# Kernel tuning notes

Hardware: AMD Instinct MI355X
Metric: run time of the kernel (lower is better)

The kernel has to match this reference:

```python
import jax, jax.numpy as jnp
import numpy as np

D_MODEL, N_HEADS, D_K, D_V, D_FF, N_LAYERS = 512, 8, 64, 64, 2048, 6
NEG = -1e9
EPS = 1e-5


def layernorm(x):
    # nn.LayerNorm(d_model) created fresh each call: weight=1, bias=0
    mu = jnp.mean(x, axis=-1, keepdims=True)
    var = jnp.var(x, axis=-1, keepdims=True)
    return (x - mu) * jax.lax.rsqrt(var + EPS)


def sinusoidal_pe(seq_len, d_model, dtype=jnp.float32):
    pos = np.arange(seq_len)[:, None].astype(np.float64)
    div = np.exp(np.arange(0, d_model, 2).astype(np.float64) * (-np.log(10000.0) / d_model))
    pe = np.zeros((seq_len, d_model))
    pe[:, 0::2] = np.sin(pos * div)
    pe[:, 1::2] = np.cos(pos * div)
    return jnp.asarray(pe, dtype=dtype)


def mha(q_in, k_in, v_in, mask, Wq, Wk, Wv, Wo):
    # q_in: [B,Lq,D]; k_in/v_in: [B,Lk,D]; mask: [B,Lq,Lk] bool (True = masked)
    B, Lq, _ = q_in.shape
    Lk = k_in.shape[1]
    Q = (q_in @ Wq).reshape(B, Lq, N_HEADS, D_K).transpose(0, 2, 1, 3)
    K = (k_in @ Wk).reshape(B, Lk, N_HEADS, D_K).transpose(0, 2, 1, 3)
    V = (v_in @ Wv).reshape(B, Lk, N_HEADS, D_V).transpose(0, 2, 1, 3)
    scores = jnp.einsum('bhqd,bhkd->bhqk', Q, K) / jnp.sqrt(jnp.asarray(D_K, q_in.dtype))
    scores = jnp.where(mask[:, None, :, :], jnp.asarray(NEG, scores.dtype), scores)
    attn = jax.nn.softmax(scores, axis=-1)
    ctx = jnp.einsum('bhqk,bhkd->bhqd', attn, V)
    ctx = ctx.transpose(0, 2, 1, 3).reshape(B, Lq, N_HEADS * D_V)
    return layernorm(ctx @ Wo + q_in)


def setup_inputs() -> dict:
    key = jax.random.key(0)
    ks = jax.random.split(key, 16)
    B, T, S, V = 8, 1024, 1024, 32000
    s = 0.02
    inp = {
        'dec_inputs': jax.random.randint(ks[0], (B, T), 0, V),
        'enc_inputs': jax.random.randint(ks[1], (B, S), 0, V),
        'enc_outputs': jax.random.normal(ks[2], (B, S, D_MODEL), jnp.float32),
        'emb': jax.random.normal(ks[3], (V, D_MODEL), jnp.float32) * s,
        'Wq_self': jax.random.normal(ks[4], (N_LAYERS, D_MODEL, N_HEADS * D_K), jnp.float32) * s,
        'Wk_self': jax.random.normal(ks[5], (N_LAYERS, D_MODEL, N_HEADS * D_K), jnp.float32) * s,
        'Wv_self': jax.random.normal(ks[6], (N_LAYERS, D_MODEL, N_HEADS * D_V), jnp.float32) * s,
        'Wo_self': jax.random.normal(ks[7], (N_LAYERS, N_HEADS * D_V, D_MODEL), jnp.float32) * s,
        'Wq_cross': jax.random.normal(ks[8], (N_LAYERS, D_MODEL, N_HEADS * D_K), jnp.float32) * s,
        'Wk_cross': jax.random.normal(ks[9], (N_LAYERS, D_MODEL, N_HEADS * D_K), jnp.float32) * s,
        'Wv_cross': jax.random.normal(ks[10], (N_LAYERS, D_MODEL, N_HEADS * D_V), jnp.float32) * s,
        'Wo_cross': jax.random.normal(ks[11], (N_LAYERS, N_HEADS * D_V, D_MODEL), jnp.float32) * s,
        'W1': jax.random.normal(ks[12], (N_LAYERS, D_MODEL, D_FF), jnp.float32) * s,
        'W2': jax.random.normal(ks[13], (N_LAYERS, D_FF, D_MODEL), jnp.float32) * s,
    }
    return inp


def reference(dec_inputs, enc_inputs, enc_outputs, emb, Wq_self, Wk_self, Wv_self, Wo_self,
              Wq_cross, Wk_cross, Wv_cross, Wo_cross, W1, W2):
    B, T = dec_inputs.shape
    S = enc_inputs.shape[1]
    # embedding with padding_idx=0 (row 0 forced to zero)
    emb_eff = emb.at[0].set(0.0)
    x = emb_eff[dec_inputs] + sinusoidal_pe(T, D_MODEL, emb.dtype)[None, :, :]
    # masks: True = masked
    pad_self = (dec_inputs == 0)[:, None, :]                       # [B,1,T]
    causal = jnp.triu(jnp.ones((T, T), bool), k=1)[None, :, :]     # [1,T,T]
    self_mask = pad_self | causal                                  # [B,T,T]
    enc_mask = jnp.broadcast_to((enc_inputs == 0)[:, None, :], (B, T, S))

    def layer(x, p):
        wqs, wks, wvs, wos, wqc, wkc, wvc, woc, w1, w2 = p
        x = mha(x, x, x, self_mask, wqs, wks, wvs, wos)
        x = mha(x, enc_outputs, enc_outputs, enc_mask, wqc, wkc, wvc, woc)
        h = jax.nn.relu(x @ w1) @ w2
        return layernorm(h + x), None

    params = (Wq_self, Wk_self, Wv_self, Wo_self, Wq_cross, Wk_cross, Wv_cross, Wo_cross, W1, W2)
    x, _ = jax.lax.scan(layer, x, params)
    return x
```

## Files before the change

kernel.cpp:

```cpp
#include <hip/hip_runtime.h>
#include <hip/hip_bf16.h>

#define DMODEL 512
#define NH     8
#define DHEAD  64
#define DFF    2048
#define NLAYER 6
#define BB     8
#define TT     1024
#define NTOK   (BB*TT)
#define ACTE   ((size_t)NTOK*DMODEL)

#define QSCALE 0.18033688011112042f

#define RESCALE_THR 8.0f

typedef __bf16  bf16x8  __attribute__((ext_vector_type(8)));
typedef float   float4v __attribute__((ext_vector_type(4)));
typedef short   short4v __attribute__((ext_vector_type(4)));
typedef short   short8v __attribute__((ext_vector_type(8)));

__device__ __forceinline__ unsigned short f2bf(float f) {
    __hip_bfloat16 h = __float2bfloat16(f);
    return *reinterpret_cast<unsigned short*>(&h);
}

__device__ __forceinline__ void gl_lds16(const void* g, void* l) {
    __builtin_amdgcn_global_load_lds((const __attribute__((address_space(1))) void*)g,
                                     (__attribute__((address_space(3))) void*)l, 16, 0, 0);
}

__device__ __forceinline__ int sigma64(int x) {
    return (x & 32) | ((x & 12) << 1) | ((x & 16) >> 2) | (x & 3);
}

struct Tr8Args {
    const float* src[8];
    unsigned short* dst[8];
    int dstL[8];
    int rowOff[8];
};
__global__ __launch_bounds__(256) void transpose8_kernel(Tr8Args a)
{
    __shared__ float tile[64][65];
    const int type = blockIdx.z / 6, lyr = blockIdx.z % 6;
    const float* src = a.src[type] + (size_t)lyr * 512 * 512;
    unsigned short* dst = a.dst[type] + (size_t)lyr * a.dstL[type];
    const int rowOff = a.rowOff[type];
    const int k0 = blockIdx.x * 64, n0 = blockIdx.y * 64;
    const int tid = threadIdx.x;
#pragma unroll
    for (int rep = 0; rep < 16; ++rep) {
        int idx = rep * 256 + tid;
        int r = idx >> 6, c = idx & 63;
        tile[r][c] = src[(size_t)(k0 + r) * 512 + n0 + c];
    }
    __syncthreads();
#pragma unroll
    for (int rep = 0; rep < 16; ++rep) {
        int idx = rep * 256 + tid;
        int r = idx >> 6, c = idx & 63;
        dst[(size_t)(rowOff + n0 + r) * 512 + k0 + c] = f2bf(tile[c][r]);
    }
}

__global__ __launch_bounds__(256) void transpose_conv_kernel(
    const float* __restrict__ W, unsigned short* __restrict__ Wt, int K, int N,
    size_t dstL, int rowOff)
{
    __shared__ float tile[64][65];
    const float* src = W + (size_t)blockIdx.z * K * N;
    unsigned short* dst = Wt + (size_t)blockIdx.z * dstL;
    const int k0 = blockIdx.x * 64, n0 = blockIdx.y * 64;
    const int tid = threadIdx.x;
#pragma unroll
    for (int rep = 0; rep < 16; ++rep) {
        int idx = rep * 256 + tid;
        int r = idx >> 6, c = idx & 63;
        tile[r][c] = src[(size_t)(k0 + r) * N + n0 + c];
    }
    __syncthreads();
#pragma unroll
    for (int rep = 0; rep < 16; ++rep) {
        int idx = rep * 256 + tid;
        int r = idx >> 6, c = idx & 63;
        dst[(size_t)(rowOff + n0 + r) * K + k0 + c] = f2bf(tile[c][r]);
    }
}

__global__ __launch_bounds__(256) void conv_bf16_kernel(
    const float* __restrict__ in, unsigned short* __restrict__ o)
{
    int i = (blockIdx.x * 256 + threadIdx.x) * 4;
    float4v v = *(const float4v*)(in + i);
    short4v w;
    w[0] = (short)f2bf(v[0]); w[1] = (short)f2bf(v[1]);
    w[2] = (short)f2bf(v[2]); w[3] = (short)f2bf(v[3]);
    *(short4v*)(o + i) = w;
}

__global__ __launch_bounds__(256) void embed_kernel(
    const int* __restrict__ dec, const float* __restrict__ emb,
    unsigned short* __restrict__ xb)
{
    const int row = blockIdx.x;
    const int t = row & (TT - 1);
    const int tid = threadIdx.x;
    const int tok = dec[row];
#pragma unroll
    for (int rep = 0; rep < 2; ++rep) {
        int c = tid + rep * 256;
        float e = (tok != 0) ? emb[(size_t)tok * DMODEL + c] : 0.f;
        int j = c >> 1;
        float freq = __expf(-(float)(2 * j) * (9.210340371976184f / 512.f));
        float ang = (float)t * freq;
        float pe = (c & 1) ? cosf(ang) : sinf(ang);
        xb[(size_t)row * DMODEL + c] = f2bf(e + pe);
    }
}

__global__ __launch_bounds__(256) void add_ln2(
    const float* __restrict__ t, unsigned short* __restrict__ xb,
    float* __restrict__ xout)
{
    const int lane = threadIdx.x & 63;
    const int row = blockIdx.x * 4 + (threadIdx.x >> 6);
    const size_t idx = (size_t)row * DMODEL + lane * 8;
    float4v t0 = *(const float4v*)(t + idx);
    float4v t1 = *(const float4v*)(t + idx + 4);
    float4v u0 = *(const float4v*)(t + ACTE + idx);
    float4v u1 = *(const float4v*)(t + ACTE + idx + 4);
    bf16x8 rb = *(const bf16x8*)(xb + idx);
    float v[8];
#pragma unroll
    for (int k = 0; k < 4; ++k) {
        v[k] = t0[k] + u0[k] + (float)rb[k];
        v[4 + k] = t1[k] + u1[k] + (float)rb[4 + k];
    }
    float s = 0.f, sq = 0.f;
#pragma unroll
    for (int k = 0; k < 8; ++k) { s += v[k]; sq += v[k] * v[k]; }
#pragma unroll
    for (int o = 1; o < 64; o <<= 1) { s += __shfl_xor(s, o); sq += __shfl_xor(sq, o); }
    float mu = s * (1.f / 512.f);
    float var = sq * (1.f / 512.f) - mu * mu;
    float rstd = rsqrtf(var + 1e-5f);
    if (xout) {
        float4v y0, y1;
#pragma unroll
        for (int k = 0; k < 4; ++k) { y0[k] = (v[k] - mu) * rstd; y1[k] = (v[4 + k] - mu) * rstd; }
        *(float4v*)(xout + idx) = y0;
        *(float4v*)(xout + idx + 4) = y1;
    } else {
        short8v w;
#pragma unroll
        for (int k = 0; k < 8; ++k) w[k] = (short)f2bf((v[k] - mu) * rstd);
        *(short8v*)(xb + idx) = w;
    }
}

template <int EPI, int SPLITK = 1>
__global__ __launch_bounds__(256) void gemm_bt(
    const unsigned short* __restrict__ A,
    const unsigned short* __restrict__ Bt,
    float* __restrict__ Cf,
    unsigned short* __restrict__ Cb,
    int M, int N, int K)
{
    __shared__ __attribute__((aligned(16))) short As[2 * 128 * 32];
    __shared__ __attribute__((aligned(16))) short Bs[2 * 128 * 32];
    const int tid = threadIdx.x;
    const int lane = tid & 63, wv = tid >> 6;
    const int quad = lane >> 4, l15 = lane & 15;
    const int m0 = blockIdx.x * 128, n0 = blockIdx.y * 128;
    const int wm = wv & 1, wn = wv >> 1;

    float4v acc[4][4];
#pragma unroll
    for (int i = 0; i < 4; ++i)
#pragma unroll
        for (int j = 0; j < 4; ++j) acc[i][j] = (float4v){0.f, 0.f, 0.f, 0.f};

    const int Kc = K / SPLITK;
    const int kbeg = (SPLITK > 1) ? (int)blockIdx.z * Kc : 0;
    for (int k0 = kbeg; k0 < kbeg + Kc; k0 += 64) {
#pragma unroll
        for (int c = 0; c < 2; ++c)
#pragma unroll
            for (int i = 0; i < 2; ++i) {
                const int inst = wv * 2 + i;
                const int row = inst * 16 + (lane >> 2);
                const int cb = (lane & 3) ^ ((row >> 1) & 3);
                gl_lds16(A + (size_t)(m0 + row) * K + k0 + c * 32 + cb * 8,
                         (char*)As + c * 8192 + inst * 1024);
                gl_lds16(Bt + (size_t)(n0 + row) * K + k0 + c * 32 + cb * 8,
                         (char*)Bs + c * 8192 + inst * 1024);
            }
        __syncthreads();
#pragma unroll
        for (int c = 0; c < 2; ++c) {
            bf16x8 a[4], b[4];
#pragma unroll
            for (int i = 0; i < 4; ++i) {
                const int r = wm * 64 + i * 16 + l15;
                const int st = quad ^ ((r >> 1) & 3);
                a[i] = *(const bf16x8*)&As[c * 4096 + r * 32 + st * 8];
            }
#pragma unroll
            for (int j = 0; j < 4; ++j) {
                const int r = wn * 64 + j * 16 + l15;
                const int st = quad ^ ((r >> 1) & 3);
                b[j] = *(const bf16x8*)&Bs[c * 4096 + r * 32 + st * 8];
            }
#pragma unroll
            for (int i = 0; i < 4; ++i)
#pragma unroll
                for (int j = 0; j < 4; ++j)
                    acc[i][j] = __builtin_amdgcn_mfma_f32_16x16x32_bf16(a[i], b[j], acc[i][j], 0, 0, 0);
        }
        __syncthreads();
    }

    const size_t zoff = (SPLITK > 1) ? (size_t)blockIdx.z * ACTE : 0;
#pragma unroll
    for (int i = 0; i < 4; ++i) {
        const int row_base = m0 + wm * 64 + i * 16 + quad * 4;
#pragma unroll
        for (int j = 0; j < 4; ++j) {
            const int col = n0 + wn * 64 + j * 16 + l15;
#pragma unroll
            for (int r = 0; r < 4; ++r) {
                const int row = row_base + r;
                const float v = acc[i][j][r];
                if (EPI == 0) {
                    Cf[zoff + (size_t)row * N + col] = v;
                } else if (EPI == 1) {
                    Cb[(size_t)row * N + col] = f2bf(fmaxf(v, 0.f));
                } else if (EPI == 2) {
                    const int which = col >> 9;
                    const float sc = (which == 0) ? QSCALE : 1.f;
                    const int b_ = row >> 10, t = row & (TT - 1);
                    const int h = (col >> 6) & 7, d = col & 63;
                    Cb[(size_t)which * ACTE + (((size_t)(b_ * NH + h)) * TT + t) * DHEAD + d] = f2bf(v * sc);
                } else {
                    const int layer = col >> 10, which = (col >> 9) & 1;
                    const int b_ = row >> 10, t = row & (TT - 1);
                    const int h = (col >> 6) & 7, d = col & 63;
                    Cb[(size_t)(layer * 2 + which) * ACTE +
                       (((size_t)(b_ * NH + h)) * TT + t) * DHEAD + d] = f2bf(v);
                }
            }
        }
    }
}

template <bool CAUSAL, int CHAINS>
__global__ __launch_bounds__(256, (CHAINS == 1 ? 4 : 2)) void attn_kernel(
    const unsigned short* __restrict__ Q,
    const unsigned short* __restrict__ Kb,
    const unsigned short* __restrict__ Vb,
    const int* __restrict__ tokens,
    unsigned short* __restrict__ ctx)
{
    __shared__ __attribute__((aligned(16))) short Ks[2][64 * 64];
    __shared__ __attribute__((aligned(16))) short Vt[2][64 * 64];

    const int tid = threadIdx.x, lane = tid & 63, wv = tid >> 6;
    const int quad = lane >> 4, l15 = lane & 15;
    const int bh = blockIdx.x;
    const int qt0 = CAUSAL ? (15 - (int)blockIdx.y) : (int)blockIdx.y;
    const int qt1 = qt0 + 8;
    const int b = bh >> 3, h = bh & 7;
    const size_t kvbase = (size_t)bh * TT * DHEAD;

    const int qcol = wv * 16 + l15;
    const int qg0 = qt0 * 64 + qcol;
    const int qg1 = qt1 * 64 + qcol;

    const bf16x8 qa0 = *(const bf16x8*)&Q[kvbase + (size_t)qg0 * DHEAD + quad * 8];
    const bf16x8 qa1 = *(const bf16x8*)&Q[kvbase + (size_t)qg0 * DHEAD + 32 + quad * 8];
    bf16x8 qb0, qb1;
    if (CHAINS == 2) {
        qb0 = *(const bf16x8*)&Q[kvbase + (size_t)qg1 * DHEAD + quad * 8];
        qb1 = *(const bf16x8*)&Q[kvbase + (size_t)qg1 * DHEAD + 32 + quad * 8];
    }

    float4v O0[4], O1[4];
#pragma unroll
    for (int j = 0; j < 4; ++j) { O0[j] = (float4v){0.f,0.f,0.f,0.f}; O1[j] = (float4v){0.f,0.f,0.f,0.f}; }
    float m0_ = -INFINITY, l0_ = 0.f, m1_ = -INFINITY, l1_ = 0.f;

    const int sig = sigma64(lane);

    const int key0 = (lane & 31) * 2;
    const int d0 = (lane >> 5) * 8 + wv * 16;
    auto stageK = [&](int kt_, int buf) {
#pragma unroll
        for (int i = 0; i < 2; ++i) {
            const int inst = wv * 2 + i;
            const int row = inst * 8 + (lane >> 3);
            const int cb = (lane & 7) ^ (row & 7);
            gl_lds16(Kb + kvbase + (size_t)(kt_ * 64 + sigma64(row)) * DHEAD + cb * 8,
                     (char*)Ks[buf] + inst * 1024);
        }
    };
    auto loadV = [&](int kt_, short8v& r0, short8v& r1) {
        const unsigned short* vp = Vb + kvbase + (size_t)(kt_ * 64 + key0) * DHEAD + d0;
        r0 = *(const short8v*)vp;
        r1 = *(const short8v*)(vp + DHEAD);
    };
    auto writeV = [&](int buf, const short8v& r0, const short8v& r1) {
        const int kc = key0 >> 3, ko = key0 & 7;
#pragma unroll
        for (int j = 0; j < 8; ++j) {
            const int d = d0 + j;
            unsigned pk = (unsigned)(unsigned short)r0[j] |
                          ((unsigned)(unsigned short)r1[j] << 16);
            *(unsigned*)&Vt[buf][d * 64 + ((kc ^ (d & 7)) << 3) + ko] = pk;
        }
    };

    auto softmax_step = [&](const float4v* st, unsigned long long kbits, bool diag,
                            float& m, float& l, float4v* O, bf16x8& p0, bf16x8& p1) {
        const bool domask = (kbits != 0ull) || diag;
        float sv[16], smax = -INFINITY;
        if (domask) {
#pragma unroll
            for (int i = 0; i < 4; ++i)
#pragma unroll
                for (int r = 0; r < 4; ++r) {
                    const int kl = i * 16 + quad * 4 + r;
                    const int klocal = sigma64(kl);
                    const bool mk = ((kbits >> kl) & 1ull) || (diag && klocal > qcol);
                    const float s = mk ? -1e9f : st[i][r];
                    sv[i * 4 + r] = s;
                    smax = fmaxf(smax, s);
                }
        } else {
#pragma unroll
            for (int i = 0; i < 4; ++i)
#pragma unroll
                for (int r = 0; r < 4; ++r) {
                    const float s = st[i][r];
                    sv[i * 4 + r] = s;
                    smax = fmaxf(smax, s);
                }
        }
        smax = fmaxf(smax, __shfl_xor(smax, 16));
        smax = fmaxf(smax, __shfl_xor(smax, 32));
        const bool resc = !__all(smax - m <= RESCALE_THR);
        const float mnew = resc ? fmaxf(m, smax) : m;
        float tsum = 0.f;
#pragma unroll
        for (int i = 0; i < 16; ++i) {
            float pv = __builtin_amdgcn_exp2f(sv[i] - mnew);
            sv[i] = pv; tsum += pv;
        }
        tsum += __shfl_xor(tsum, 16);
        tsum += __shfl_xor(tsum, 32);
        short8v pw0, pw1;
#pragma unroll
        for (int t = 0; t < 8; ++t) {
            pw0[t] = (short)f2bf(sv[t]);
            pw1[t] = (short)f2bf(sv[8 + t]);
        }
        p0 = *reinterpret_cast<const bf16x8*>(&pw0);
        p1 = *reinterpret_cast<const bf16x8*>(&pw1);
        if (resc) {
            const float alpha = __builtin_amdgcn_exp2f(m - mnew);
            l = l * alpha + tsum;
            m = mnew;
            float4v av;
#pragma unroll
            for (int r = 0; r < 4; ++r) av[r] = __shfl(alpha, quad * 4 + r);
#pragma unroll
            for (int j = 0; j < 4; ++j) O[j] = O[j] * av;
        } else {
            l += tsum;
        }
    };

    const int nkt = CAUSAL ? (qt0 + 1) : 16;

    stageK(0, 0);
    {
        short8v v0a, v0b;
        loadV(0, v0a, v0b);
        writeV(0, v0a, v0b);
    }
    int tok_cur = tokens[(size_t)b * TT + sig];
    __syncthreads();

    short8v vn0, vn1;
    int tok_next = 0;
    for (int kt = 0; kt < nkt; ++kt) {
        const int cur = kt & 1, nxt = cur ^ 1;
        const bool more = (kt + 1 < nkt);
        if (more) {
            stageK(kt + 1, nxt);
            loadV(kt + 1, vn0, vn1);
            tok_next = tokens[(size_t)b * TT + (kt + 1) * 64 + sig];
        }
        const unsigned long long kbits = __ballot(tok_cur == 0);

        if (CHAINS == 1) {
            float4v st[4];
            __builtin_amdgcn_s_setprio(1);
#pragma unroll
            for (int i = 0; i < 4; ++i) {
                const int row = i * 16 + l15;
                const int x = row & 7;
                const bf16x8 k0 = *(const bf16x8*)&Ks[cur][row * 64 + ((quad ^ x)) * 8];
                const bf16x8 k1 = *(const bf16x8*)&Ks[cur][row * 64 + (((4 + quad) ^ x)) * 8];
                float4v z = (float4v){0.f, 0.f, 0.f, 0.f};
                z = __builtin_amdgcn_mfma_f32_16x16x32_bf16(k0, qa0, z, 0, 0, 0);
                z = __builtin_amdgcn_mfma_f32_16x16x32_bf16(k1, qa1, z, 0, 0, 0);
                st[i] = z;
            }
            __builtin_amdgcn_s_setprio(0);
            bf16x8 p0, p1;
            softmax_step(st, kbits, CAUSAL && (kt == qt0), m0_, l0_, O0, p0, p1);
            __builtin_amdgcn_s_setprio(1);
#pragma unroll
            for (int j = 0; j < 4; ++j) {
                const int row = j * 16 + l15;
                const int x = row & 7;
                const bf16x8 v0 = *(const bf16x8*)&Vt[cur][row * 64 + ((quad ^ x)) * 8];
                const bf16x8 v1 = *(const bf16x8*)&Vt[cur][row * 64 + (((4 + quad) ^ x)) * 8];
                float4v o = O0[j];
                o = __builtin_amdgcn_mfma_f32_16x16x32_bf16(p0, v0, o, 0, 0, 0);
                o = __builtin_amdgcn_mfma_f32_16x16x32_bf16(p1, v1, o, 0, 0, 0);
                O0[j] = o;
            }
            __builtin_amdgcn_s_setprio(0);
        } else {
            bf16x8 kf[4][2], vf[4][2];
#pragma unroll
            for (int i = 0; i < 4; ++i) {
                const int row = i * 16 + l15;
                const int x = row & 7;
                kf[i][0] = *(const bf16x8*)&Ks[cur][row * 64 + ((quad ^ x)) * 8];
                kf[i][1] = *(const bf16x8*)&Ks[cur][row * 64 + (((4 + quad) ^ x)) * 8];
                vf[i][0] = *(const bf16x8*)&Vt[cur][row * 64 + ((quad ^ x)) * 8];
                vf[i][1] = *(const bf16x8*)&Vt[cur][row * 64 + (((4 + quad) ^ x)) * 8];
            }
#pragma unroll
            for (int ch = 0; ch < 2; ++ch) {
                const bf16x8& qf0 = ch ? qb0 : qa0;
                const bf16x8& qf1 = ch ? qb1 : qa1;
                float& m = ch ? m1_ : m0_;
                float& l = ch ? l1_ : l0_;
                float4v* O = ch ? O1 : O0;
                float4v st[4];
                __builtin_amdgcn_s_setprio(1);
#pragma unroll
                for (int i = 0; i < 4; ++i) {
                    float4v z = (float4v){0.f, 0.f, 0.f, 0.f};
                    z = __builtin_amdgcn_mfma_f32_16x16x32_bf16(kf[i][0], qf0, z, 0, 0, 0);
                    z = __builtin_amdgcn_mfma_f32_16x16x32_bf16(kf[i][1], qf1, z, 0, 0, 0);
                    st[i] = z;
                }
                __builtin_amdgcn_s_setprio(0);
                bf16x8 p0, p1;
                softmax_step(st, kbits, false, m, l, O, p0, p1);
                __builtin_amdgcn_s_setprio(1);
#pragma unroll
                for (int j = 0; j < 4; ++j) {
                    float4v o = O[j];
                    o = __builtin_amdgcn_mfma_f32_16x16x32_bf16(p0, vf[j][0], o, 0, 0, 0);
                    o = __builtin_amdgcn_mfma_f32_16x16x32_bf16(p1, vf[j][1], o, 0, 0, 0);
                    O[j] = o;
                }
                __builtin_amdgcn_s_setprio(0);
            }
        }

        if (more) {
            writeV(nxt, vn0, vn1);
            tok_cur = tok_next;
        }
        __syncthreads();
    }

    auto finalize = [&](float l, float4v* O, int qt) {
        float4v lw;
#pragma unroll
        for (int r = 0; r < 4; ++r) lw[r] = __shfl(l, quad * 4 + r);
        float rl[4];
#pragma unroll
        for (int r = 0; r < 4; ++r) rl[r] = __builtin_amdgcn_rcpf(lw[r]);
#pragma unroll
        for (int j = 0; j < 4; ++j)
#pragma unroll
            for (int r = 0; r < 4; ++r) {
                const int qrow = qt * 64 + wv * 16 + quad * 4 + r;
                ctx[((size_t)b * TT + qrow) * DMODEL + h * DHEAD + j * 16 + l15] =
                    f2bf(O[j][r] * rl[r]);
            }
    };
    finalize(l0_, O0, qt0);
    if (CHAINS == 2) finalize(l1_, O1, qt1);
}

extern "C" void kernel_launch(void* const* d_in, const int* in_sizes, int n_in,
                              void* d_out, int out_size, void* d_ws, size_t ws_size,
                              hipStream_t stream)
{
    const int* dec = (const int*)d_in[0];
    const int* enc = (const int*)d_in[1];
    const float* enc_out = (const float*)d_in[2];
    const float* emb = (const float*)d_in[3];
    const float* Wq_s = (const float*)d_in[4];
    const float* Wk_s = (const float*)d_in[5];
    const float* Wv_s = (const float*)d_in[6];
    const float* Wo_s = (const float*)d_in[7];
    const float* Wq_c = (const float*)d_in[8];
    const float* Wk_c = (const float*)d_in[9];
    const float* Wv_c = (const float*)d_in[10];
    const float* Wo_c = (const float*)d_in[11];
    const float* W1 = (const float*)d_in[12];
    const float* W2 = (const float*)d_in[13];
    float* out = (float*)d_out;

    char* p = (char*)d_ws;
    auto carve = [&](size_t bytes) -> char* {
        char* r = p;
        p += (bytes + 255) & ~(size_t)255;
        return r;
    };
    unsigned short* xb   = (unsigned short*)carve(ACTE * 2);
    float* tmp1          = (float*)carve(2 * ACTE * 4);
    unsigned short* qkvb = (unsigned short*)carve(3 * ACTE * 2);
    unsigned short* ctxb = (unsigned short*)carve(ACTE * 2);
    unsigned short* encb = (unsigned short*)carve(ACTE * 2);
    unsigned short* h1   = (unsigned short*)carve((size_t)NTOK * DFF * 2);
    unsigned short* wqkvT = (unsigned short*)carve((size_t)NLAYER * 1536 * 512 * 2);
    unsigned short* woT   = (unsigned short*)carve((size_t)NLAYER * 512 * 512 * 2);
    unsigned short* wqcT  = (unsigned short*)carve((size_t)NLAYER * 512 * 512 * 2);
    unsigned short* wkvcT = (unsigned short*)carve((size_t)NLAYER * 1024 * 512 * 2);
    unsigned short* wocT  = (unsigned short*)carve((size_t)NLAYER * 512 * 512 * 2);
    unsigned short* w1T   = (unsigned short*)carve((size_t)NLAYER * 2048 * 512 * 2);
    unsigned short* w2T   = (unsigned short*)carve((size_t)NLAYER * 512 * 2048 * 2);
    const size_t used = (size_t)(p - (char*)d_ws);
    const bool pre = (used + 12 * ACTE * 2 + 256) <= ws_size;
    unsigned short* KVc = pre ? (unsigned short*)carve(12 * ACTE * 2) : nullptr;

    Tr8Args ta;
    ta.src[0] = Wq_s; ta.dst[0] = wqkvT; ta.dstL[0] = 1536 * 512; ta.rowOff[0] = 0;
    ta.src[1] = Wk_s; ta.dst[1] = wqkvT; ta.dstL[1] = 1536 * 512; ta.rowOff[1] = 512;
    ta.src[2] = Wv_s; ta.dst[2] = wqkvT; ta.dstL[2] = 1536 * 512; ta.rowOff[2] = 1024;
    ta.src[3] = Wo_s; ta.dst[3] = woT;   ta.dstL[3] = 512 * 512;  ta.rowOff[3] = 0;
    ta.src[4] = Wq_c; ta.dst[4] = wqcT;  ta.dstL[4] = 512 * 512;  ta.rowOff[4] = 0;
    ta.src[5] = Wk_c; ta.dst[5] = wkvcT; ta.dstL[5] = 1024 * 512; ta.rowOff[5] = 0;
    ta.src[6] = Wv_c; ta.dst[6] = wkvcT; ta.dstL[6] = 1024 * 512; ta.rowOff[6] = 512;
    ta.src[7] = Wo_c; ta.dst[7] = wocT;  ta.dstL[7] = 512 * 512;  ta.rowOff[7] = 0;
    transpose8_kernel<<<dim3(8, 8, 48), 256, 0, stream>>>(ta);
    transpose_conv_kernel<<<dim3(8, 32, NLAYER), 256, 0, stream>>>(W1, w1T, 512, 2048, (size_t)2048 * 512, 0);
    transpose_conv_kernel<<<dim3(32, 8, NLAYER), 256, 0, stream>>>(W2, w2T, 2048, 512, (size_t)512 * 2048, 0);
    conv_bf16_kernel<<<(int)(ACTE / 1024), 256, 0, stream>>>(enc_out, encb);
    embed_kernel<<<NTOK, 256, 0, stream>>>(dec, emb, xb);

    if (pre)
        gemm_bt<3><<<dim3(64, 48), 256, 0, stream>>>(encb, wkvcT, nullptr, KVc, NTOK, 6144, 512);

    for (int lyr = 0; lyr < NLAYER; ++lyr) {
        const unsigned short* wqkv = wqkvT + (size_t)lyr * 1536 * 512;
        const unsigned short* wo   = woT + (size_t)lyr * 512 * 512;
        const unsigned short* wqc  = wqcT + (size_t)lyr * 512 * 512;
        const unsigned short* wkvc = wkvcT + (size_t)lyr * 1024 * 512;
        const unsigned short* woc  = wocT + (size_t)lyr * 512 * 512;
        const unsigned short* w1   = w1T + (size_t)lyr * 2048 * 512;
        const unsigned short* w2   = w2T + (size_t)lyr * 512 * 2048;

        gemm_bt<2><<<dim3(64, 12), 256, 0, stream>>>(xb, wqkv, nullptr, qkvb, NTOK, 1536, 512);
        attn_kernel<true, 1><<<dim3(BB * NH, 16), 256, 0, stream>>>(
            qkvb, qkvb + ACTE, qkvb + 2 * ACTE, dec, ctxb);
        gemm_bt<0, 2><<<dim3(64, 4, 2), 256, 0, stream>>>(ctxb, wo, tmp1, nullptr, NTOK, 512, 512);
        add_ln2<<<NTOK / 4, 256, 0, stream>>>(tmp1, xb, nullptr);

        gemm_bt<2><<<dim3(64, 4), 256, 0, stream>>>(xb, wqc, nullptr, qkvb, NTOK, 512, 512);
        const unsigned short* Kc;
        if (pre) {
            Kc = KVc + (size_t)lyr * 2 * ACTE;
        } else {
            gemm_bt<2><<<dim3(64, 8), 256, 0, stream>>>(encb, wkvc, nullptr, qkvb + ACTE, NTOK, 1024, 512);
            Kc = qkvb + ACTE;
        }
        attn_kernel<false, 2><<<dim3(BB * NH, 8), 256, 0, stream>>>(
            qkvb, Kc, Kc + ACTE, enc, ctxb);
        gemm_bt<0, 2><<<dim3(64, 4, 2), 256, 0, stream>>>(ctxb, woc, tmp1, nullptr, NTOK, 512, 512);
        add_ln2<<<NTOK / 4, 256, 0, stream>>>(tmp1, xb, nullptr);

        gemm_bt<1><<<dim3(64, 16), 256, 0, stream>>>(xb, w1, nullptr, h1, NTOK, 2048, 512);
        gemm_bt<0, 2><<<dim3(64, 4, 2), 256, 0, stream>>>(h1, w2, tmp1, nullptr, NTOK, 512, 2048);
        add_ln2<<<NTOK / 4, 256, 0, stream>>>(tmp1, xb, (lyr == NLAYER - 1) ? out : nullptr);
    }
    (void)in_sizes; (void)n_in; (void)out_size;
}
```

Baseline: 1.475 ms.

## Double-buffer GEMM K-tiles and reorder causal attention tile scheduling

The bf16 GEMM now works on 32-wide K slices held in two LDS buffers. The next slice is prefetched into the idle buffer while MFMAs run on the current one, so there is a single barrier per slice instead of a load-sync-compute-sync sequence. This is meant to hide global-to-LDS latency behind compute, at the cost of more barriers per unit of K work. Causal attention blocks also get a new interleaved query-tile order, mixing heavy and light tiles to even out work across CUs.

```diff
diff --git a/kernel.cpp b/kernel.cpp
--- a/kernel.cpp
+++ b/kernel.cpp
@@ -167,8 +167,8 @@
     unsigned short* __restrict__ Cb,
     int M, int N, int K)
 {
-    __shared__ __attribute__((aligned(16))) short As[2 * 128 * 32];
-    __shared__ __attribute__((aligned(16))) short Bs[2 * 128 * 32];
+    __shared__ __attribute__((aligned(16))) short As[2][128 * 32];
+    __shared__ __attribute__((aligned(16))) short Bs[2][128 * 32];
     const int tid = threadIdx.x;
     const int lane = tid & 63, wv = tid >> 6;
     const int quad = lane >> 4, l15 = lane & 15;
@@ -183,41 +183,42 @@
 
     const int Kc = K / SPLITK;
     const int kbeg = (SPLITK > 1) ? (int)blockIdx.z * Kc : 0;
-    for (int k0 = kbeg; k0 < kbeg + Kc; k0 += 64) {
-#pragma unroll
-        for (int c = 0; c < 2; ++c)
-#pragma unroll
-            for (int i = 0; i < 2; ++i) {
-                const int inst = wv * 2 + i;
-                const int row = inst * 16 + (lane >> 2);
-                const int cb = (lane & 3) ^ ((row >> 1) & 3);
-                gl_lds16(A + (size_t)(m0 + row) * K + k0 + c * 32 + cb * 8,
-                         (char*)As + c * 8192 + inst * 1024);
-                gl_lds16(Bt + (size_t)(n0 + row) * K + k0 + c * 32 + cb * 8,
-                         (char*)Bs + c * 8192 + inst * 1024);
-            }
-        __syncthreads();
-#pragma unroll
-        for (int c = 0; c < 2; ++c) {
-            bf16x8 a[4], b[4];
-#pragma unroll
-            for (int i = 0; i < 4; ++i) {
-                const int r = wm * 64 + i * 16 + l15;
-                const int st = quad ^ ((r >> 1) & 3);
-                a[i] = *(const bf16x8*)&As[c * 4096 + r * 32 + st * 8];
-            }
-#pragma unroll
-            for (int j = 0; j < 4; ++j) {
-                const int r = wn * 64 + j * 16 + l15;
-                const int st = quad ^ ((r >> 1) & 3);
-                b[j] = *(const bf16x8*)&Bs[c * 4096 + r * 32 + st * 8];
-            }
-#pragma unroll
-            for (int i = 0; i < 4; ++i)
-#pragma unroll
-                for (int j = 0; j < 4; ++j)
-                    acc[i][j] = __builtin_amdgcn_mfma_f32_16x16x32_bf16(a[i], b[j], acc[i][j], 0, 0, 0);
-        }
+    const int kend = kbeg + Kc;
+
+    auto stage = [&](int k0, int buf) {
+#pragma unroll
+        for (int i = 0; i < 2; ++i) {
+            const int inst = wv * 2 + i;
+            const int row = inst * 16 + (lane >> 2);
+            const int cb = (lane & 3) ^ ((row >> 1) & 3);
+            gl_lds16(A + (size_t)(m0 + row) * K + k0 + cb * 8, (char*)As[buf] + inst * 1024);
+            gl_lds16(Bt + (size_t)(n0 + row) * K + k0 + cb * 8, (char*)Bs[buf] + inst * 1024);
+        }
+    };
+
+    stage(kbeg, 0);
+    __syncthreads();
+    for (int k0 = kbeg; k0 < kend; k0 += 32) {
+        const int buf = ((k0 - kbeg) >> 5) & 1;
+        if (k0 + 32 < kend) stage(k0 + 32, buf ^ 1);
+        bf16x8 a[4], b[4];
+#pragma unroll
+        for (int i = 0; i < 4; ++i) {
+            const int r = wm * 64 + i * 16 + l15;
+            const int st = quad ^ ((r >> 1) & 3);
+            a[i] = *(const bf16x8*)&As[buf][r * 32 + st * 8];
+        }
+#pragma unroll
+        for (int j = 0; j < 4; ++j) {
+            const int r = wn * 64 + j * 16 + l15;
+            const int st = quad ^ ((r >> 1) & 3);
+            b[j] = *(const bf16x8*)&Bs[buf][r * 32 + st * 8];
+        }
+#pragma unroll
+        for (int i = 0; i < 4; ++i)
+#pragma unroll
+            for (int j = 0; j < 4; ++j)
+                acc[i][j] = __builtin_amdgcn_mfma_f32_16x16x32_bf16(a[i], b[j], acc[i][j], 0, 0, 0);
         __syncthreads();
     }
 
@@ -268,7 +269,13 @@
     const int tid = threadIdx.x, lane = tid & 63, wv = tid >> 6;
     const int quad = lane >> 4, l15 = lane & 15;
     const int bh = blockIdx.x;
-    const int qt0 = CAUSAL ? (15 - (int)blockIdx.y) : (int)blockIdx.y;
+    int qt0;
+    if (CAUSAL) {
+        const int y = blockIdx.y, grp = y >> 2, r = y & 3;
+        qt0 = (grp == 0) ? 15 - r : (grp == 1) ? r : (grp == 2) ? 11 - r : 4 + r;
+    } else {
+        qt0 = blockIdx.y;
+    }
     const int qt1 = qt0 + 8;
     const int b = bh >> 3, h = bh & 7;
     const size_t kvbase = (size_t)bh * TT * DHEAD;
```

Result: slower. 1.537 ms (+4.2%).

## Pair causal query tiles per block to balance work and share K/V fragments

Applied to the files above, without the earlier changes.

The causal self-attention kernel now processes two query tiles per block, tile y and its mirror 15-y, so every block does the same total number of key tiles. The K and V LDS fragments loaded for each key tile are reused across both query chains, and chain 0 skips key tiles beyond its diagonal. This halves the grid, evens out per-block load and cuts LDS reads per query. The cost is higher register pressure, with launch bounds dropped from 4 to 2 blocks per CU, and less parallelism in flight.

```diff
diff --git a/kernel.cpp b/kernel.cpp
--- a/kernel.cpp
+++ b/kernel.cpp
@@ -254,8 +254,8 @@
     }
 }
 
-template <bool CAUSAL, int CHAINS>
-__global__ __launch_bounds__(256, (CHAINS == 1 ? 4 : 2)) void attn_kernel(
+template <bool CAUSAL>
+__global__ __launch_bounds__(256, 2) void attn_kernel(
     const unsigned short* __restrict__ Q,
     const unsigned short* __restrict__ Kb,
     const unsigned short* __restrict__ Vb,
@@ -268,8 +268,8 @@
     const int tid = threadIdx.x, lane = tid & 63, wv = tid >> 6;
     const int quad = lane >> 4, l15 = lane & 15;
     const int bh = blockIdx.x;
-    const int qt0 = CAUSAL ? (15 - (int)blockIdx.y) : (int)blockIdx.y;
-    const int qt1 = qt0 + 8;
+    const int qt0 = blockIdx.y;
+    const int qt1 = CAUSAL ? (15 - qt0) : (qt0 + 8);
     const int b = bh >> 3, h = bh & 7;
     const size_t kvbase = (size_t)bh * TT * DHEAD;
 
@@ -279,11 +279,8 @@
 
     const bf16x8 qa0 = *(const bf16x8*)&Q[kvbase + (size_t)qg0 * DHEAD + quad * 8];
     const bf16x8 qa1 = *(const bf16x8*)&Q[kvbase + (size_t)qg0 * DHEAD + 32 + quad * 8];
-    bf16x8 qb0, qb1;
-    if (CHAINS == 2) {
-        qb0 = *(const bf16x8*)&Q[kvbase + (size_t)qg1 * DHEAD + quad * 8];
-        qb1 = *(const bf16x8*)&Q[kvbase + (size_t)qg1 * DHEAD + 32 + quad * 8];
-    }
+    const bf16x8 qb0 = *(const bf16x8*)&Q[kvbase + (size_t)qg1 * DHEAD + quad * 8];
+    const bf16x8 qb1 = *(const bf16x8*)&Q[kvbase + (size_t)qg1 * DHEAD + 32 + quad * 8];
 
     float4v O0[4], O1[4];
 #pragma unroll
@@ -320,7 +317,7 @@
         }
     };
 
-    auto softmax_step = [&](const float4v* st, unsigned long long kbits, bool diag,
+    auto softmax_step = [&](const float4v* st, unsigned long long kbits, bool diag, int qc,
                             float& m, float& l, float4v* O, bf16x8& p0, bf16x8& p1) {
         const bool domask = (kbits != 0ull) || diag;
         float sv[16], smax = -INFINITY;
@@ -331,7 +328,7 @@
                 for (int r = 0; r < 4; ++r) {
                     const int kl = i * 16 + quad * 4 + r;
                     const int klocal = sigma64(kl);
-                    const bool mk = ((kbits >> kl) & 1ull) || (diag && klocal > qcol);
+                    const bool mk = ((kbits >> kl) & 1ull) || (diag && klocal > qc);
                     const float s = mk ? -1e9f : st[i][r];
                     sv[i * 4 + r] = s;
                     smax = fmaxf(smax, s);
@@ -380,7 +377,7 @@
         }
     };
 
-    const int nkt = CAUSAL ? (qt0 + 1) : 16;
+    const int nkt = CAUSAL ? (qt1 + 1) : 16;
 
     stageK(0, 0);
     {
@@ -403,76 +400,46 @@
         }
         const unsigned long long kbits = __ballot(tok_cur == 0);
 
-        if (CHAINS == 1) {
+        bf16x8 kf[4][2], vf[4][2];
+#pragma unroll
+        for (int i = 0; i < 4; ++i) {
+            const int row = i * 16 + l15;
+            const int x = row & 7;
+            kf[i][0] = *(const bf16x8*)&Ks[cur][row * 64 + ((quad ^ x)) * 8];
+            kf[i][1] = *(const bf16x8*)&Ks[cur][row * 64 + (((4 + quad) ^ x)) * 8];
+            vf[i][0] = *(const bf16x8*)&Vt[cur][row * 64 + ((quad ^ x)) * 8];
+            vf[i][1] = *(const bf16x8*)&Vt[cur][row * 64 + (((4 + quad) ^ x)) * 8];
+        }
+#pragma unroll
+        for (int ch = 0; ch < 2; ++ch) {
+            const int qtc = ch ? qt1 : qt0;
+            if (CAUSAL && ch == 0 && kt > qt0) continue;
+            const bf16x8& qf0 = ch ? qb0 : qa0;
+            const bf16x8& qf1 = ch ? qb1 : qa1;
+            float& m = ch ? m1_ : m0_;
+            float& l = ch ? l1_ : l0_;
+            float4v* O = ch ? O1 : O0;
             float4v st[4];
             __builtin_amdgcn_s_setprio(1);
 #pragma unroll
             for (int i = 0; i < 4; ++i) {
-                const int row = i * 16 + l15;
-                const int x = row & 7;
-                const bf16x8 k0 = *(const bf16x8*)&Ks[cur][row * 64 + ((quad ^ x)) * 8];
-                const bf16x8 k1 = *(const bf16x8*)&Ks[cur][row * 64 + (((4 + quad) ^ x)) * 8];
                 float4v z = (float4v){0.f, 0.f, 0.f, 0.f};
-                z = __builtin_amdgcn_mfma_f32_16x16x32_bf16(k0, qa0, z, 0, 0, 0);
-                z = __builtin_amdgcn_mfma_f32_16x16x32_bf16(k1, qa1, z, 0, 0, 0);
+                z = __builtin_amdgcn_mfma_f32_16x16x32_bf16(kf[i][0], qf0, z, 0, 0, 0);
+                z = __builtin_amdgcn_mfma_f32_16x16x32_bf16(kf[i][1], qf1, z, 0, 0, 0);
                 st[i] = z;
             }
             __builtin_amdgcn_s_setprio(0);
             bf16x8 p0, p1;
-            softmax_step(st, kbits, CAUSAL && (kt == qt0), m0_, l0_, O0, p0, p1);
+            softmax_step(st, kbits, CAUSAL && (kt == qtc), qcol, m, l, O, p0, p1);
             __builtin_amdgcn_s_setprio(1);
 #pragma unroll
             for (int j = 0; j < 4; ++j) {
-                const int row = j * 16 + l15;
-                const int x = row & 7;
-                const bf16x8 v0 = *(const bf16x8*)&Vt[cur][row * 64 + ((quad ^ x)) * 8];
-                const bf16x8 v1 = *(const bf16x8*)&Vt[cur][row * 64 + (((4 + quad) ^ x)) * 8];
-                float4v o = O0[j];
-                o = __builtin_amdgcn_mfma_f32_16x16x32_bf16(p0, v0, o, 0, 0, 0);
-                o = __builtin_amdgcn_mfma_f32_16x16x32_bf16(p1, v1, o, 0, 0, 0);
-                O0[j] = o;
+                float4v o = O[j];
+                o = __builtin_amdgcn_mfma_f32_16x16x32_bf16(p0, vf[j][0], o, 0, 0, 0);
+                o = __builtin_amdgcn_mfma_f32_16x16x32_bf16(p1, vf[j][1], o, 0, 0, 0);
+                O[j] = o;
             }
             __builtin_amdgcn_s_setprio(0);
-        } else {
-            bf16x8 kf[4][2], vf[4][2];
-#pragma unroll
-            for (int i = 0; i < 4; ++i) {
-                const int row = i * 16 + l15;
-                const int x = row & 7;
-                kf[i][0] = *(const bf16x8*)&Ks[cur][row * 64 + ((quad ^ x)) * 8];
-                kf[i][1] = *(const bf16x8*)&Ks[cur][row * 64 + (((4 + quad) ^ x)) * 8];
-                vf[i][0] = *(const bf16x8*)&Vt[cur][row * 64 + ((quad ^ x)) * 8];
-                vf[i][1] = *(const bf16x8*)&Vt[cur][row * 64 + (((4 + quad) ^ x)) * 8];
-            }
-#pragma unroll
-            for (int ch = 0; ch < 2; ++ch) {
-                const bf16x8& qf0 = ch ? qb0 : qa0;
-                const bf16x8& qf1 = ch ? qb1 : qa1;
-                float& m = ch ? m1_ : m0_;
-                float& l = ch ? l1_ : l0_;
-                float4v* O = ch ? O1 : O0;
-                float4v st[4];
-                __builtin_amdgcn_s_setprio(1);
-#pragma unroll
-                for (int i = 0; i < 4; ++i) {
-                    float4v z = (float4v){0.f, 0.f, 0.f, 0.f};
-                    z = __builtin_amdgcn_mfma_f32_16x16x32_bf16(kf[i][0], qf0, z, 0, 0, 0);
-                    z = __builtin_amdgcn_mfma_f32_16x16x32_bf16(kf[i][1], qf1, z, 0, 0, 0);
-                    st[i] = z;
-                }
-                __builtin_amdgcn_s_setprio(0);
-                bf16x8 p0, p1;
-                softmax_step(st, kbits, false, m, l, O, p0, p1);
-                __builtin_amdgcn_s_setprio(1);
-#pragma unroll
-                for (int j = 0; j < 4; ++j) {
-                    float4v o = O[j];
-                    o = __builtin_amdgcn_mfma_f32_16x16x32_bf16(p0, vf[j][0], o, 0, 0, 0);
-                    o = __builtin_amdgcn_mfma_f32_16x16x32_bf16(p1, vf[j][1], o, 0, 0, 0);
-                    O[j] = o;
-                }
-                __builtin_amdgcn_s_setprio(0);
-            }
         }
 
         if (more) {
@@ -499,7 +466,7 @@
             }
     };
     finalize(l0_, O0, qt0);
-    if (CHAINS == 2) finalize(l1_, O1, qt1);
+    finalize(l1_, O1, qt1);
 }
 
 extern "C" void kernel_launch(void* const* d_in, const int* in_sizes, int n_in,
@@ -573,7 +540,7 @@
         const unsigned short* w2   = w2T + (size_t)lyr * 512 * 2048;
 
         gemm_bt<2><<<dim3(64, 12), 256, 0, stream>>>(xb, wqkv, nullptr, qkvb, NTOK, 1536, 512);
-        attn_kernel<true, 1><<<dim3(BB * NH, 16), 256, 0, stream>>>(
+        attn_kernel<true><<<dim3(BB * NH, 8), 256, 0, stream>>>(
             qkvb, qkvb + ACTE, qkvb + 2 * ACTE, dec, ctxb);
         gemm_bt<0, 2><<<dim3(64, 4, 2), 256, 0, stream>>>(ctxb, wo, tmp1, nullptr, NTOK, 512, 512);
         add_ln2<<<NTOK / 4, 256, 0, stream>>>(tmp1, xb, nullptr);
@@ -586,7 +553,7 @@
             gemm_bt<2><<<dim3(64, 8), 256, 0, stream>>>(encb, wkvc, nullptr, qkvb + ACTE, NTOK, 1024, 512);
             Kc = qkvb + ACTE;
         }
-        attn_kernel<false, 2><<<dim3(BB * NH, 8), 256, 0, stream>>>(
+        attn_kernel<false><<<dim3(BB * NH, 8), 256, 0, stream>>>(
             qkvb, Kc, Kc + ACTE, enc, ctxb);
         gemm_bt<0, 2><<<dim3(64, 4, 2), 256, 0, stream>>>(ctxb, woc, tmp1, nullptr, NTOK, 512, 512);
         add_ln2<<<NTOK / 4, 256, 0, stream>>>(tmp1, xb, nullptr);
```

New measurement: 1.494 ms. Within noise of the previous version (+1.3%).
